# Kernel tuning notes

Measured on AMD Instinct MI355X. Metric: run time of the kernel, lower is better.

The kernel has to match this reference:

```python
import jax, jax.numpy as jnp
import numpy as np

D_MODEL = 256; N_HEADS = 8; N_LEVELS = 4; N_POINTS = 4; D_FFN = 1024
BS = 8; NQ = 100; NKPT = 17
LEVEL_SHAPES = [(160, 160), (80, 80), (40, 40), (20, 20)]  # (H, W) per level
LEN_V = sum(h * w for h, w in LEVEL_SHAPES)  # 34000


def layer_norm(x, g, b, eps=1e-5):
    m = x.mean(-1, keepdims=True)
    v = ((x - m) ** 2).mean(-1, keepdims=True)
    return (x - m) * jax.lax.rsqrt(v + eps) * g + b


def mha(q, k, v, Wqkv, bqkv, Wo, bo):
    # torch nn.MultiheadAttention, batch_first, eval mode (no dropout)
    d = q.shape[-1]; dh = d // N_HEADS
    def proj(x, W, b):
        return (x @ W.T + b).reshape(*x.shape[:-1], N_HEADS, dh)
    qp = proj(q, Wqkv[:d], bqkv[:d])
    kp = proj(k, Wqkv[d:2 * d], bqkv[d:2 * d])
    vp = proj(v, Wqkv[2 * d:], bqkv[2 * d:])
    att = jnp.einsum('bqhd,bkhd->bhqk', qp, kp) / jnp.sqrt(jnp.asarray(dh, q.dtype))
    att = jax.nn.softmax(att, -1)
    out = jnp.einsum('bhqk,bkhd->bqhd', att, vp).reshape(q.shape)
    return out @ Wo.T + bo


def bilinear_sample(val, loc, h, w):
    # val: (B, H, h*w, Dh); loc: (B, Lq, H, P, 2) normalized to [0,1]
    # matches F.grid_sample(align_corners=False, padding_mode='zeros') on grid 2*loc-1
    B, Lq, H, P, _ = loc.shape
    px = loc[..., 0] * w - 0.5
    py = loc[..., 1] * h - 0.5
    x0f = jnp.floor(px); y0f = jnp.floor(py)
    lx = px - x0f; ly = py - y0f
    x0 = x0f.astype(jnp.int32); y0 = y0f.astype(jnp.int32)
    out = jnp.zeros((B, H, Lq, P, val.shape[-1]), val.dtype)
    for dx, dy, wt in ((0, 0, (1 - lx) * (1 - ly)), (1, 0, lx * (1 - ly)),
                       (0, 1, (1 - lx) * ly), (1, 1, lx * ly)):
        xi = x0 + dx; yi = y0 + dy
        valid = ((xi >= 0) & (xi < w) & (yi >= 0) & (yi < h)).astype(val.dtype)
        idx = jnp.clip(yi, 0, h - 1) * w + jnp.clip(xi, 0, w - 1)  # (B,Lq,H,P)
        idx = idx.transpose(0, 2, 1, 3).reshape(B, H, Lq * P)
        g = jnp.take_along_axis(val, idx[..., None], axis=2).reshape(B, H, Lq, P, -1)
        out = out + g * (wt * valid).transpose(0, 2, 1, 3)[..., None]
    return out  # (B, H, Lq, P, Dh)


def ms_deform_attn(query, ref_points, memory, off_W, off_b, aw_W, aw_b,
                   val_W, val_b, outp_W, outp_b):
    B, Lq, _ = query.shape
    dh = D_MODEL // N_HEADS
    value = (memory @ val_W.T + val_b).reshape(B, LEN_V, N_HEADS, dh)
    off = (query @ off_W.T + off_b).reshape(B, Lq, N_HEADS, N_LEVELS, N_POINTS, 2)
    aw = (query @ aw_W.T + aw_b).reshape(B, Lq, N_HEADS, N_LEVELS * N_POINTS)
    aw = jax.nn.softmax(aw, -1).reshape(B, Lq, N_HEADS, N_LEVELS, N_POINTS)
    normalizer = jnp.array([[w, h] for h, w in LEVEL_SHAPES], dtype=query.dtype)  # (L,2) as (W,H)
    loc = ref_points[:, :, None, :, None, :] + off / normalizer[None, None, None, :, None, :]
    out = jnp.zeros((B, Lq, N_HEADS, dh), query.dtype)
    start = 0
    for l, (h, w) in enumerate(LEVEL_SHAPES):
        vl = value[:, start:start + h * w].transpose(0, 2, 1, 3)  # (B,H,hw,Dh)
        s = bilinear_sample(vl, loc[:, :, :, l], h, w)            # (B,H,Lq,P,Dh)
        out = out + jnp.einsum('bhqpd,bqhp->bqhd', s, aw[:, :, :, l])
        start += h * w
    return out.reshape(B, Lq, D_MODEL) @ outp_W.T + outp_b


def setup_inputs() -> dict:
    key = jax.random.key(0)
    ks = iter(jax.random.split(key, 40))
    d = D_MODEL
    def w(shape, s=0.02):
        return jax.random.normal(next(ks), shape, jnp.float32) * s
    inp = {
        'tgt_pose': jax.random.normal(next(ks), (BS, NQ, NKPT, d), jnp.float32),
        'tgt_pose_query_pos': jax.random.normal(next(ks), (BS, NQ, NKPT, d), jnp.float32),
        'tgt_pose_reference_points': jax.random.uniform(next(ks), (BS, NQ * NKPT, N_LEVELS, 2), jnp.float32),
        'memory': jax.random.normal(next(ks), (BS, LEN_V, d), jnp.float32),
        'win_Wqkv': w((3 * d, d)), 'win_bqkv': jnp.zeros((3 * d,), jnp.float32),
        'win_Wo': w((d, d)), 'win_bo': jnp.zeros((d,), jnp.float32),
        'win_ng': jnp.ones((d,), jnp.float32), 'win_nb': jnp.zeros((d,), jnp.float32),
        'acr_Wqkv': w((3 * d, d)), 'acr_bqkv': jnp.zeros((3 * d,), jnp.float32),
        'acr_Wo': w((d, d)), 'acr_bo': jnp.zeros((d,), jnp.float32),
        'acr_ng': jnp.ones((d,), jnp.float32), 'acr_nb': jnp.zeros((d,), jnp.float32),
        'off_W': w((N_HEADS * N_LEVELS * N_POINTS * 2, d)),
        'off_b': jax.random.uniform(next(ks), (N_HEADS * N_LEVELS * N_POINTS * 2,), jnp.float32, -1.0, 1.0),
        'aw_W': w((N_HEADS * N_LEVELS * N_POINTS, d)), 'aw_b': jnp.zeros((N_HEADS * N_LEVELS * N_POINTS,), jnp.float32),
        'val_W': w((d, d)), 'val_b': jnp.zeros((d,), jnp.float32),
        'outp_W': w((d, d)), 'outp_b': jnp.zeros((d,), jnp.float32),
        'gate_W': w((2 * d, 2 * d)), 'gate_b': jnp.zeros((2 * d,), jnp.float32),
        'gate_ng': jnp.ones((d,), jnp.float32), 'gate_nb': jnp.zeros((d,), jnp.float32),
        'ffn_W1': w((D_FFN, d)), 'ffn_b1': jnp.zeros((D_FFN,), jnp.float32),
        'ffn_W2': w((d, D_FFN)), 'ffn_b2': jnp.zeros((d,), jnp.float32),
        'n2_g': jnp.ones((d,), jnp.float32), 'n2_b': jnp.zeros((d,), jnp.float32),
        'memory_spatial_shapes': jnp.array(LEVEL_SHAPES, jnp.int32),
    }
    return inp


def reference(tgt_pose, tgt_pose_query_pos, tgt_pose_reference_points, memory,
              win_Wqkv, win_bqkv, win_Wo, win_bo, win_ng, win_nb,
              acr_Wqkv, acr_bqkv, acr_Wo, acr_bo, acr_ng, acr_nb,
              off_W, off_b, aw_W, aw_b, val_W, val_b, outp_W, outp_b,
              gate_W, gate_b, gate_ng, gate_nb,
              ffn_W1, ffn_b1, ffn_W2, ffn_b2, n2_g, n2_b,
              memory_spatial_shapes):
    bs, nq, K, d = tgt_pose.shape
    # with_pos_embed mutates tgt_pose in place in the torch code -> residual includes pos
    tgt = tgt_pose + tgt_pose_query_pos
    # within-attention over keypoints of each query
    x = tgt.reshape(bs * nq, K, d)
    t2 = mha(x, x, x, win_Wqkv, win_bqkv, win_Wo, win_bo).reshape(bs, nq, K, d)
    tgt = layer_norm(tgt + t2, win_ng, win_nb)
    # across-attention over queries for each keypoint
    xk = tgt.transpose(0, 2, 1, 3).reshape(bs * K, nq, d)
    t2 = mha(xk, xk, xk, acr_Wqkv, acr_bqkv, acr_Wo, acr_bo)
    tgt = layer_norm(xk + t2, acr_ng, acr_nb).reshape(bs, K, nq, d).transpose(0, 2, 1, 3)
    # second in-place pos add before deformable cross-attn (also feeds gateway)
    tgt_q = tgt + tgt_pose_query_pos
    t2 = ms_deform_attn(tgt_q.reshape(bs, nq * K, d), tgt_pose_reference_points, memory,
                        off_W, off_b, aw_W, aw_b, val_W, val_b, outp_W, outp_b)
    t2 = t2.reshape(bs, nq, K, d)
    # Gate
    g = jax.nn.sigmoid(jnp.concatenate([tgt_q, t2], -1) @ gate_W.T + gate_b)
    g1, g2 = jnp.split(g, 2, -1)
    tgt = layer_norm(g1 * tgt_q + g2 * t2, gate_ng, gate_nb)
    # FFN
    h = jax.nn.relu(tgt @ ffn_W1.T + ffn_b1)
    tgt = tgt + h @ ffn_W2.T + ffn_b2
    tgt = layer_norm(jnp.clip(tgt, -65504.0, 65504.0), n2_g, n2_b)
    return tgt
```

## Files before the change

kernel.cpp:

```cpp
#include <hip/hip_runtime.h>
#include <hip/hip_bf16.h>

#define NH 8
#define BS_ 8
#define NQ_ 100
#define NK_ 17
#define LQ 1700
#define T_TOK 13600
#define LEN_VV 34000

typedef __attribute__((ext_vector_type(8))) short short8v;
typedef __attribute__((ext_vector_type(8))) __bf16 bf16x8;
typedef __attribute__((ext_vector_type(4))) float f32x4;

__device__ __forceinline__ float wave_sum(float v){
#pragma unroll
  for (int m = 32; m; m >>= 1) v += __shfl_xor(v, m, 64);
  return v;
}
__device__ __forceinline__ short f2bf(float f){
  __hip_bfloat16 h = __float2bfloat16(f);
  return *reinterpret_cast<short*>(&h);
}

__global__ __launch_bounds__(256) void add_k(const float* __restrict__ a,
                                             const float* __restrict__ b,
                                             float* __restrict__ o, int n4){
  int i = blockIdx.x * 256 + threadIdx.x;
  if (i >= n4) return;
  float4 x = ((const float4*)a)[i];
  float4 y = ((const float4*)b)[i];
  float4 r; r.x = x.x + y.x; r.y = x.y + y.y; r.z = x.z + y.z; r.w = x.w + y.w;
  ((float4*)o)[i] = r;
}

__global__ __launch_bounds__(256) void transpose_k(const float* __restrict__ in,
                                                   float* __restrict__ outp){
  int i = blockIdx.x * 256 + threadIdx.x;
  if (i >= T_TOK * 64) return;
  int orow = i >> 6, c = i & 63;
  int b = orow / LQ, rem = orow % LQ;
  int kk = rem / NQ_, q = rem % NQ_;
  int irow = b * LQ + q * NK_ + kk;
  ((float4*)outp)[(size_t)orow * 64 + c] = ((const float4*)in)[(size_t)irow * 64 + c];
}

__global__ __launch_bounds__(256) void concat_k(const float* __restrict__ a,
                                                const float* __restrict__ b,
                                                float* __restrict__ o){
  int i = blockIdx.x * 256 + threadIdx.x;
  if (i >= T_TOK * 128) return;
  int row = i >> 7, c = i & 127;
  float4 v = (c < 64) ? ((const float4*)a)[(size_t)row * 64 + c]
                      : ((const float4*)b)[(size_t)row * 64 + (c - 64)];
  ((float4*)o)[(size_t)row * 128 + c] = v;
}

template<int EPI, int OUTB>
__global__ __launch_bounds__(256) void mgemm_k(const float* __restrict__ A,
                                               const float* __restrict__ W,
                                               const float* __restrict__ bias,
                                               float* __restrict__ Cf,
                                               __hip_bfloat16* __restrict__ Cb,
                                               int M, int N, int K){
  __shared__ short sh[OUTB ? 128 * 136 : 128 * 128];
  short* As = sh;
  short* Ws = sh + 128 * 64;
  const int tid = threadIdx.x;
  const int bm = blockIdx.y * 128, bn = blockIdx.x * 128;
  const int wave = tid >> 6, lane = tid & 63;
  const int wm = (wave >> 1) * 64, wn = (wave & 1) * 64;
  const int s = tid & 7;
  const int row0 = tid >> 3;
  f32x4 acc[4][4] = {};
  const int lrow = lane & 15, lk = lane >> 4;

  float4 ra[8], rw[8];
#pragma unroll
  for (int i = 0; i < 4; i++){
    int row = row0 + i * 32;
    int gr = bm + row;
    float4 z = make_float4(0.f, 0.f, 0.f, 0.f);
    if (gr < M){
      const float* p = A + (size_t)gr * K + s * 8;
      ra[2 * i] = ((const float4*)p)[0]; ra[2 * i + 1] = ((const float4*)p)[1];
    } else { ra[2 * i] = z; ra[2 * i + 1] = z; }
    const float* q = W + (size_t)(bn + row) * K + s * 8;
    rw[2 * i] = ((const float4*)q)[0]; rw[2 * i + 1] = ((const float4*)q)[1];
  }

  for (int k0 = 0; k0 < K; k0 += 64){
#pragma unroll
    for (int i = 0; i < 4; i++){
      int row = row0 + i * 32;
      int sw = ((s ^ (row & 7)) << 3) + row * 64;
      float4 a0 = ra[2 * i], a1 = ra[2 * i + 1];
      short8v v;
      v[0]=f2bf(a0.x); v[1]=f2bf(a0.y); v[2]=f2bf(a0.z); v[3]=f2bf(a0.w);
      v[4]=f2bf(a1.x); v[5]=f2bf(a1.y); v[6]=f2bf(a1.z); v[7]=f2bf(a1.w);
      *(short8v*)&As[sw] = v;
      a0 = rw[2 * i]; a1 = rw[2 * i + 1];
      short8v u;
      u[0]=f2bf(a0.x); u[1]=f2bf(a0.y); u[2]=f2bf(a0.z); u[3]=f2bf(a0.w);
      u[4]=f2bf(a1.x); u[5]=f2bf(a1.y); u[6]=f2bf(a1.z); u[7]=f2bf(a1.w);
      *(short8v*)&Ws[sw] = u;
    }
    __syncthreads();
    if (k0 + 64 < K){
#pragma unroll
      for (int i = 0; i < 4; i++){
        int row = row0 + i * 32;
        int gr = bm + row;
        float4 z = make_float4(0.f, 0.f, 0.f, 0.f);
        if (gr < M){
          const float* p = A + (size_t)gr * K + k0 + 64 + s * 8;
          ra[2 * i] = ((const float4*)p)[0]; ra[2 * i + 1] = ((const float4*)p)[1];
        } else { ra[2 * i] = z; ra[2 * i + 1] = z; }
        const float* q = W + (size_t)(bn + row) * K + k0 + 64 + s * 8;
        rw[2 * i] = ((const float4*)q)[0]; rw[2 * i + 1] = ((const float4*)q)[1];
      }
    }
#pragma unroll
    for (int ks = 0; ks < 2; ks++){
      short8v af[4], bw[4];
      int slot = ks * 4 + lk;
#pragma unroll
      for (int m = 0; m < 4; m++){
        int r = wm + m * 16 + lrow;
        af[m] = *(const short8v*)&As[r * 64 + ((slot ^ (r & 7)) << 3)];
      }
#pragma unroll
      for (int n = 0; n < 4; n++){
        int r = wn + n * 16 + lrow;
        bw[n] = *(const short8v*)&Ws[r * 64 + ((slot ^ (r & 7)) << 3)];
      }
#pragma unroll
      for (int m = 0; m < 4; m++)
#pragma unroll
        for (int n = 0; n < 4; n++)
          acc[m][n] = __builtin_amdgcn_mfma_f32_16x16x32_bf16(
              __builtin_bit_cast(bf16x8, af[m]),
              __builtin_bit_cast(bf16x8, bw[n]), acc[m][n], 0, 0, 0);
    }
    __syncthreads();
  }
  if (OUTB){
    const int STR = 136;
#pragma unroll
    for (int n = 0; n < 4; n++){
      int col = wn + n * 16 + lrow;
      float bsv = bias[bn + col];
#pragma unroll
      for (int m = 0; m < 4; m++){
#pragma unroll
        for (int i = 0; i < 4; i++){
          int row = wm + m * 16 + lk * 4 + i;
          float c = acc[m][n][i] + bsv;
          if (EPI == 1) c = fmaxf(c, 0.f);
          if (EPI == 2) c = 1.f / (1.f + expf(-c));
          sh[row * STR + col] = f2bf(c);
        }
      }
    }
    __syncthreads();
#pragma unroll
    for (int it = 0; it < 8; it++){
      int r = it * 16 + (tid >> 4);
      int chunk = tid & 15;
      if (bm + r < M){
        uint4 v = *(const uint4*)((const char*)sh + r * 272 + chunk * 16);
        *(uint4*)((char*)Cb + ((size_t)(bm + r) * N + bn) * 2 + chunk * 16) = v;
      }
    }
  } else {
#pragma unroll
    for (int n = 0; n < 4; n++){
      int col = bn + wn + n * 16 + lrow;
      float bsv = bias[col];
#pragma unroll
      for (int m = 0; m < 4; m++){
#pragma unroll
        for (int i = 0; i < 4; i++){
          int row = bm + wm + m * 16 + lk * 4 + i;
          if (row >= M) continue;
          float c = acc[m][n][i] + bsv;
          if (EPI == 1) c = fmaxf(c, 0.f);
          if (EPI == 2) c = 1.f / (1.f + expf(-c));
          Cf[(size_t)row * N + col] = c;
        }
      }
    }
  }
}

template<int TP>
__global__ __launch_bounds__(256) void mha_mfma_k(const float* __restrict__ qkv,
                                                  float* __restrict__ out, int S){
  constexpr int MT = TP / 16;
  constexpr int KSTEPS = (TP + 31) / 32;
  constexpr int KS32 = KSTEPS * 32;
  constexpr int VSTRB = (KS32 == 128) ? 256 : 128;
  __shared__ short QK[2][TP][64];
  __shared__ short Vt[2][32][VSTRB / 2];
  __shared__ float Sc[2][16][128];
  __shared__ float rinv[2][16];

  const int tid = threadIdx.x;
  const int bid = blockIdx.x;
  const int batch = bid >> 2, hp = bid & 3;
  const int wave = tid >> 6, lane = tid & 63;
  const int hh = wave >> 1, wsub = wave & 1;
  const int lrow = lane & 15, lk = lane >> 4;
  const float scale = 0.17677669529663687f;
  const size_t qbase = (size_t)batch * S * 768;

  for (int idx = tid; idx < 2 * TP * 4; idx += 256){
    int h2 = idx >= TP * 4;
    int rem = idx - h2 * TP * 4;
    int j = rem >> 2, s = rem & 3;
    int h = hp * 2 + h2;
    short8v qv = {}, kv = {};
    if (j < S){
      const float* p = qkv + qbase + (size_t)j * 768 + h * 32 + s * 8;
      float4 a = ((const float4*)p)[0];
      float4 b = ((const float4*)p)[1];
      qv[0]=f2bf(a.x*scale); qv[1]=f2bf(a.y*scale); qv[2]=f2bf(a.z*scale); qv[3]=f2bf(a.w*scale);
      qv[4]=f2bf(b.x*scale); qv[5]=f2bf(b.y*scale); qv[6]=f2bf(b.z*scale); qv[7]=f2bf(b.w*scale);
      float4 c = ((const float4*)(p + 256))[0];
      float4 d = ((const float4*)(p + 256))[1];
      kv[0]=f2bf(c.x); kv[1]=f2bf(c.y); kv[2]=f2bf(c.z); kv[3]=f2bf(c.w);
      kv[4]=f2bf(d.x); kv[5]=f2bf(d.y); kv[6]=f2bf(d.z); kv[7]=f2bf(d.w);
    }
    *(short8v*)&QK[h2][j][(s ^ (j & 7)) << 3] = qv;
    *(short8v*)&QK[h2][j][((s + 4) ^ (j & 7)) << 3] = kv;
  }
  for (int idx = tid; idx < 2 * KS32 * 8; idx += 256){
    int h2 = idx >= KS32 * 8;
    int rem = idx - h2 * KS32 * 8;
    int j = rem >> 3, e4 = rem & 7;
    int h = hp * 2 + h2;
    float4 v = make_float4(0.f, 0.f, 0.f, 0.f);
    if (j < S) v = *(const float4*)(qkv + qbase + (size_t)j * 768 + h * 32 + 512 + e4 * 4);
    short vs4[4] = { f2bf(v.x), f2bf(v.y), f2bf(v.z), f2bf(v.w) };
#pragma unroll
    for (int c = 0; c < 4; c++){
      int e = e4 * 4 + c;
      char* pb = (char*)&Vt[h2][0][0] + e * VSTRB + (((j >> 3) ^ (e & 7)) << 4) + ((j & 7) << 1);
      *(short*)pb = vs4[c];
    }
  }
  __syncthreads();

  for (int mt = 0; mt < MT; mt++){
    for (int nt = wsub; nt < MT; nt += 2){
      int ar = mt * 16 + lrow;
      short8v aq = *(const short8v*)&QK[hh][ar][(lk ^ (ar & 7)) << 3];
      int br = nt * 16 + lrow;
      short8v bk = *(const short8v*)&QK[hh][br][((lk + 4) ^ (br & 7)) << 3];
      f32x4 z = {};
      f32x4 d = __builtin_amdgcn_mfma_f32_16x16x32_bf16(
          __builtin_bit_cast(bf16x8, aq), __builtin_bit_cast(bf16x8, bk), z, 0, 0, 0);
#pragma unroll
      for (int i = 0; i < 4; i++){
        int rr = lk * 4 + i;
        int c = nt * 16 + lrow;
        Sc[hh][rr][(((c >> 2) ^ (rr & 7)) << 2) + (c & 3)] = d[i];
      }
    }
    __syncthreads();
    if (wsub == 0){
      int rr = lane >> 2, p = lane & 3;
      int grow = mt * 16 + rr;
      int Seff = (grow < S) ? S : 0;
      float mx = -1e30f;
#pragma unroll
      for (int m = 0; m < KSTEPS; m++){
        int j = p + 4 * m;
#pragma unroll
        for (int half = 0; half < 2; half++){
          int ls = 2 * j + half;
          float4 v = *(const float4*)&Sc[hh][rr][(ls ^ (rr & 7)) << 2];
          int c0 = ls * 4;
          mx = fmaxf(mx, (c0 + 0 < Seff) ? v.x : -1e30f);
          mx = fmaxf(mx, (c0 + 1 < Seff) ? v.y : -1e30f);
          mx = fmaxf(mx, (c0 + 2 < Seff) ? v.z : -1e30f);
          mx = fmaxf(mx, (c0 + 3 < Seff) ? v.w : -1e30f);
        }
      }
      mx = fmaxf(mx, __shfl_xor(mx, 1, 64));
      mx = fmaxf(mx, __shfl_xor(mx, 2, 64));
      float sum = 0.f;
#pragma unroll
      for (int m = 0; m < KSTEPS; m++){
        int j = p + 4 * m;
        float ev[8];
#pragma unroll
        for (int half = 0; half < 2; half++){
          int ls = 2 * j + half;
          float4 v = *(const float4*)&Sc[hh][rr][(ls ^ (rr & 7)) << 2];
          int c0 = ls * 4;
          ev[half * 4 + 0] = (c0 + 0 < Seff) ? __expf(v.x - mx) : 0.f;
          ev[half * 4 + 1] = (c0 + 1 < Seff) ? __expf(v.y - mx) : 0.f;
          ev[half * 4 + 2] = (c0 + 2 < Seff) ? __expf(v.z - mx) : 0.f;
          ev[half * 4 + 3] = (c0 + 3 < Seff) ? __expf(v.w - mx) : 0.f;
        }
        short8v pb;
#pragma unroll
        for (int q2 = 0; q2 < 8; q2++){ pb[q2] = f2bf(ev[q2]); sum += ev[q2]; }
        *(short8v*)((char*)&Sc[hh][rr][0] + ((j ^ (rr & 7)) << 4)) = pb;
      }
      sum += __shfl_xor(sum, 1, 64);
      sum += __shfl_xor(sum, 2, 64);
      if (p == 0) rinv[hh][rr] = (sum > 0.f) ? 1.f / sum : 0.f;
    }
    __syncthreads();
    {
      int nt2 = wsub;
      f32x4 acc = {};
#pragma unroll
      for (int ks = 0; ks < KSTEPS; ks++){
        int slot = ks * 4 + lk;
        short8v ap = *(const short8v*)((const char*)&Sc[hh][lrow][0] + ((slot ^ (lrow & 7)) << 4));
        int e = nt2 * 16 + lrow;
        short8v bv = *(const short8v*)((const char*)&Vt[hh][0][0] + e * VSTRB + ((slot ^ (e & 7)) << 4));
        acc = __builtin_amdgcn_mfma_f32_16x16x32_bf16(
            __builtin_bit_cast(bf16x8, ap), __builtin_bit_cast(bf16x8, bv), acc, 0, 0, 0);
      }
      int h = hp * 2 + hh;
#pragma unroll
      for (int i = 0; i < 4; i++){
        int row = mt * 16 + lk * 4 + i;
        if (row < S){
          float rv = rinv[hh][lk * 4 + i];
          out[((size_t)batch * S + row) * 256 + h * 32 + nt2 * 16 + lrow] = acc[i] * rv;
        }
      }
    }
    __syncthreads();
  }
}

template<int MODE>
__global__ __launch_bounds__(64) void ln_k(const float* __restrict__ a,
                                           const float* __restrict__ b,
                                           const float* __restrict__ g,
                                           const float* __restrict__ be,
                                           float* __restrict__ out){
  int r = blockIdx.x;
  int lane = threadIdx.x;
  float4 xa = *(const float4*)(a + (size_t)r * 256 + lane * 4);
  float4 xb = *(const float4*)(b + (size_t)r * 256 + lane * 4);
  float x[4] = { xa.x + xb.x, xa.y + xb.y, xa.z + xb.z, xa.w + xb.w };
  if (MODE == 2){
#pragma unroll
    for (int i = 0; i < 4; i++) x[i] = fminf(fmaxf(x[i], -65504.f), 65504.f);
  }
  float s = x[0] + x[1] + x[2] + x[3];
  s = wave_sum(s);
  float mean = s * (1.f / 256.f);
  float sq = 0.f;
#pragma unroll
  for (int i = 0; i < 4; i++){ float d = x[i] - mean; sq += d * d; }
  float var = wave_sum(sq) * (1.f / 256.f);
  float rstd = rsqrtf(var + 1e-5f);
  float4 gg = *(const float4*)(g + lane * 4);
  float4 bb = *(const float4*)(be + lane * 4);
  size_t orow = r;
  if (MODE == 1){
    int bi = r / LQ; int rem = r % LQ; int kk = rem / NQ_; int q = rem % NQ_;
    orow = (size_t)bi * LQ + q * NK_ + kk;
  }
  float4 o;
  o.x = (x[0] - mean) * rstd * gg.x + bb.x;
  o.y = (x[1] - mean) * rstd * gg.y + bb.y;
  o.z = (x[2] - mean) * rstd * gg.z + bb.z;
  o.w = (x[3] - mean) * rstd * gg.w + bb.w;
  *(float4*)(out + orow * 256 + lane * 4) = o;
}

__global__ __launch_bounds__(64) void gate_ln_k(const float* __restrict__ G,
                                                const float* __restrict__ aq,
                                                const float* __restrict__ t2,
                                                const float* __restrict__ g,
                                                const float* __restrict__ be,
                                                float* __restrict__ out){
  int r = blockIdx.x;
  int lane = threadIdx.x;
  float4 g1 = *(const float4*)(G + (size_t)r * 512 + lane * 4);
  float4 g2 = *(const float4*)(G + (size_t)r * 512 + 256 + lane * 4);
  float4 xa = *(const float4*)(aq + (size_t)r * 256 + lane * 4);
  float4 xt = *(const float4*)(t2 + (size_t)r * 256 + lane * 4);
  float x[4] = { g1.x * xa.x + g2.x * xt.x, g1.y * xa.y + g2.y * xt.y,
                 g1.z * xa.z + g2.z * xt.z, g1.w * xa.w + g2.w * xt.w };
  float s = x[0] + x[1] + x[2] + x[3];
  s = wave_sum(s);
  float mean = s * (1.f / 256.f);
  float sq = 0.f;
#pragma unroll
  for (int i = 0; i < 4; i++){ float d = x[i] - mean; sq += d * d; }
  float var = wave_sum(sq) * (1.f / 256.f);
  float rstd = rsqrtf(var + 1e-5f);
  float4 gg = *(const float4*)(g + lane * 4);
  float4 bb = *(const float4*)(be + lane * 4);
  float4 o;
  o.x = (x[0] - mean) * rstd * gg.x + bb.x;
  o.y = (x[1] - mean) * rstd * gg.y + bb.y;
  o.z = (x[2] - mean) * rstd * gg.z + bb.z;
  o.w = (x[3] - mean) * rstd * gg.w + bb.w;
  *(float4*)(out + (size_t)r * 256 + lane * 4) = o;
}

__global__ __launch_bounds__(256) void deform_k(const __hip_bfloat16* __restrict__ val,
                                                const float* __restrict__ off,
                                                const float* __restrict__ awr,
                                                const float* __restrict__ ref,
                                                float* __restrict__ out){
  __shared__ uint2 meta[32][16][4];
  const int tid = threadIdx.x;
  const int t0 = blockIdx.x * 4;
  {
    int g = tid >> 3;
    int pair = tid & 7;
    int lt = g >> 3, h = g & 7;
    int t = t0 + lt;
    int b = t / LQ;
    int p0 = pair * 2;
    int l = p0 >> 2;
    const int starts[4] = {0, 25600, 32000, 33600};
    const int HS[4] = {160, 80, 40, 20};
    int w = HS[l];
    float a0 = awr[(size_t)t * 128 + h * 16 + p0];
    float a1 = awr[(size_t)t * 128 + h * 16 + p0 + 1];
    float mx = fmaxf(a0, a1);
#pragma unroll
    for (int m = 1; m <= 4; m <<= 1) mx = fmaxf(mx, __shfl_xor(mx, m, 64));
    float e0 = expf(a0 - mx), e1 = expf(a1 - mx);
    float s = e0 + e1;
#pragma unroll
    for (int m = 1; m <= 4; m <<= 1) s += __shfl_xor(s, m, 64);
    float inv = 1.f / s;
    float rx = ref[((size_t)t * 4 + l) * 2 + 0];
    float ry = ref[((size_t)t * 4 + l) * 2 + 1];
    float4 ov = *(const float4*)(off + (size_t)t * 256 + h * 32 + l * 8 + p0 * 2);
    int vbase = (b * LEN_VV + starts[l]) * 128 + h * 16;
#pragma unroll
    for (int pp = 0; pp < 2; pp++){
      float wgt = (pp ? e1 : e0) * inv;
      float px = rx * w + (pp ? ov.z : ov.x) - 0.5f;
      float py = ry * w + (pp ? ov.w : ov.y) - 0.5f;
      float x0f = floorf(px), y0f = floorf(py);
      float lx = px - x0f, ly = py - y0f;
      int x0 = (int)x0f, y0 = (int)y0f;
#pragma unroll
      for (int c = 0; c < 4; c++){
        int dx = c & 1, dy = c >> 1;
        int xi = x0 + dx, yi = y0 + dy;
        bool ok = (xi >= 0) & (xi < w) & (yi >= 0) & (yi < w);
        float cw = ok ? wgt * (dx ? lx : 1.f - lx) * (dy ? ly : 1.f - ly) : 0.f;
        uint idx = ok ? (uint)(vbase + (yi * w + xi) * 128) : 0u;
        uint2 m2; m2.x = idx; m2.y = __float_as_uint(cw);
        meta[g][p0 + pp][c] = m2;
      }
    }
  }
  __syncthreads();
  const uint* V2 = (const uint*)val;
  int sg = tid >> 4, lane = tid & 15;
#pragma unroll
  for (int it = 0; it < 2; it++){
    int g = it * 16 + sg;
    int lt = g >> 3, h = g & 7;
    int t = t0 + lt;
    float ax = 0.f, ay = 0.f;
#pragma unroll 4
    for (int c = 0; c < 64; c++){
      uint2 mw = meta[g][c >> 2][c & 3];
      float wv = __uint_as_float(mw.y);
      uint v = V2[(size_t)mw.x + lane];
      float lo = __uint_as_float(v << 16);
      float hi = __uint_as_float(v & 0xffff0000u);
      ax += wv * lo;
      ay += wv * hi;
    }
    float2 r; r.x = ax; r.y = ay;
    *(float2*)(out + (size_t)t * 256 + h * 32 + lane * 2) = r;
  }
}

extern "C" void kernel_launch(void* const* d_in, const int* in_sizes, int n_in,
                              void* d_out, int out_size, void* d_ws, size_t ws_size,
                              hipStream_t stream){
  const float* tgt_pose = (const float*)d_in[0];
  const float* qpos     = (const float*)d_in[1];
  const float* refp     = (const float*)d_in[2];
  const float* memory   = (const float*)d_in[3];
  const float* win_Wqkv = (const float*)d_in[4];
  const float* win_bqkv = (const float*)d_in[5];
  const float* win_Wo   = (const float*)d_in[6];
  const float* win_bo   = (const float*)d_in[7];
  const float* win_ng   = (const float*)d_in[8];
  const float* win_nb   = (const float*)d_in[9];
  const float* acr_Wqkv = (const float*)d_in[10];
  const float* acr_bqkv = (const float*)d_in[11];
  const float* acr_Wo   = (const float*)d_in[12];
  const float* acr_bo   = (const float*)d_in[13];
  const float* acr_ng   = (const float*)d_in[14];
  const float* acr_nb   = (const float*)d_in[15];
  const float* off_W    = (const float*)d_in[16];
  const float* off_b    = (const float*)d_in[17];
  const float* aw_W     = (const float*)d_in[18];
  const float* aw_b     = (const float*)d_in[19];
  const float* val_W    = (const float*)d_in[20];
  const float* val_b    = (const float*)d_in[21];
  const float* outp_W   = (const float*)d_in[22];
  const float* outp_b   = (const float*)d_in[23];
  const float* gate_W   = (const float*)d_in[24];
  const float* gate_b   = (const float*)d_in[25];
  const float* gate_ng  = (const float*)d_in[26];
  const float* gate_nb  = (const float*)d_in[27];
  const float* ffn_W1   = (const float*)d_in[28];
  const float* ffn_b1   = (const float*)d_in[29];
  const float* ffn_W2   = (const float*)d_in[30];
  const float* ffn_b2   = (const float*)d_in[31];
  const float* n2_g     = (const float*)d_in[32];
  const float* n2_b     = (const float*)d_in[33];

  float* out = (float*)d_out;
  char* ws = (char*)d_ws;
  const size_t TB = (size_t)T_TOK * 256 * 4;
  float* B0 = (float*)(ws);
  float* B1 = (float*)(ws + TB);
  float* B2 = (float*)(ws + 2 * TB);
  float* B3 = (float*)(ws + 3 * TB);
  float* Q  = (float*)(ws + 4 * TB);
  float* AW = (float*)(ws + 4 * TB + (size_t)T_TOK * 768 * 4);
  char*  Vb = ws + 4 * TB + (size_t)T_TOK * 768 * 4 + (size_t)T_TOK * 128 * 4;
  __hip_bfloat16* V = (__hip_bfloat16*)Vb;
  float* CAT = (float*)Vb;
  float* FF  = (float*)(Vb + (size_t)T_TOK * 512 * 4);

  const int n4 = T_TOK * 64;
  const int GM = (T_TOK + 127) / 128;

  add_k<<<(n4 + 255) / 256, 256, 0, stream>>>(tgt_pose, qpos, B0, n4);
  mgemm_k<0,0><<<dim3(6, GM), 256, 0, stream>>>(B0, win_Wqkv, win_bqkv, Q, nullptr, T_TOK, 768, 256);
  mha_mfma_k<32><<<800 * 4, 256, 0, stream>>>(Q, B1, 17);
  mgemm_k<0,0><<<dim3(2, GM), 256, 0, stream>>>(B1, win_Wo, win_bo, B2, nullptr, T_TOK, 256, 256);
  ln_k<0><<<T_TOK, 64, 0, stream>>>(B0, B2, win_ng, win_nb, B1);
  transpose_k<<<(n4 + 255) / 256, 256, 0, stream>>>(B1, B0);
  mgemm_k<0,0><<<dim3(6, GM), 256, 0, stream>>>(B0, acr_Wqkv, acr_bqkv, Q, nullptr, T_TOK, 768, 256);
  mha_mfma_k<112><<<136 * 4, 256, 0, stream>>>(Q, B2, 100);
  mgemm_k<0,0><<<dim3(2, GM), 256, 0, stream>>>(B2, acr_Wo, acr_bo, B3, nullptr, T_TOK, 256, 256);
  ln_k<1><<<T_TOK, 64, 0, stream>>>(B0, B3, acr_ng, acr_nb, B1);
  add_k<<<(n4 + 255) / 256, 256, 0, stream>>>(B1, qpos, B0, n4);
  mgemm_k<0,1><<<dim3(2, 2125), 256, 0, stream>>>(memory, val_W, val_b, nullptr, V, BS_ * LEN_VV, 256, 256);
  mgemm_k<0,0><<<dim3(2, GM), 256, 0, stream>>>(B0, off_W, off_b, B1, nullptr, T_TOK, 256, 256);
  mgemm_k<0,0><<<dim3(1, GM), 256, 0, stream>>>(B0, aw_W, aw_b, AW, nullptr, T_TOK, 128, 256);
  deform_k<<<T_TOK / 4, 256, 0, stream>>>(V, B1, AW, refp, B2);
  mgemm_k<0,0><<<dim3(2, GM), 256, 0, stream>>>(B2, outp_W, outp_b, B3, nullptr, T_TOK, 256, 256);
  concat_k<<<(T_TOK * 128 + 255) / 256, 256, 0, stream>>>(B0, B3, CAT);
  mgemm_k<2,0><<<dim3(4, GM), 256, 0, stream>>>(CAT, gate_W, gate_b, Q, nullptr, T_TOK, 512, 512);
  gate_ln_k<<<T_TOK, 64, 0, stream>>>(Q, B0, B3, gate_ng, gate_nb, B1);
  mgemm_k<1,0><<<dim3(8, GM), 256, 0, stream>>>(B1, ffn_W1, ffn_b1, FF, nullptr, T_TOK, 1024, 256);
  mgemm_k<0,0><<<dim3(2, GM), 256, 0, stream>>>(FF, ffn_W2, ffn_b2, B2, nullptr, T_TOK, 256, 1024);
  ln_k<2><<<T_TOK, 64, 0, stream>>>(B1, B2, n2_g, n2_b, out);
}
```

Before: 571.2 us.

## Fuse transposes, concat and projections; use bf16 intermediates and 64-tile GEMMs

```diff
diff --git a/kernel.cpp b/kernel.cpp
--- a/kernel.cpp
+++ b/kernel.cpp
@@ -21,6 +21,9 @@
 __device__ __forceinline__ short f2bf(float f){
   __hip_bfloat16 h = __float2bfloat16(f);
   return *reinterpret_cast<short*>(&h);
+}
+__device__ __forceinline__ float bf2f(short s){
+  return __uint_as_float(((uint)(unsigned short)s) << 16);
 }
 
 __global__ __launch_bounds__(256) void add_k(const float* __restrict__ a,
@@ -32,28 +35,6 @@
   float4 y = ((const float4*)b)[i];
   float4 r; r.x = x.x + y.x; r.y = x.y + y.y; r.z = x.z + y.z; r.w = x.w + y.w;
   ((float4*)o)[i] = r;
-}
-
-__global__ __launch_bounds__(256) void transpose_k(const float* __restrict__ in,
-                                                   float* __restrict__ outp){
-  int i = blockIdx.x * 256 + threadIdx.x;
-  if (i >= T_TOK * 64) return;
-  int orow = i >> 6, c = i & 63;
-  int b = orow / LQ, rem = orow % LQ;
-  int kk = rem / NQ_, q = rem % NQ_;
-  int irow = b * LQ + q * NK_ + kk;
-  ((float4*)outp)[(size_t)orow * 64 + c] = ((const float4*)in)[(size_t)irow * 64 + c];
-}
-
-__global__ __launch_bounds__(256) void concat_k(const float* __restrict__ a,
-                                                const float* __restrict__ b,
-                                                float* __restrict__ o){
-  int i = blockIdx.x * 256 + threadIdx.x;
-  if (i >= T_TOK * 128) return;
-  int row = i >> 7, c = i & 127;
-  float4 v = (c < 64) ? ((const float4*)a)[(size_t)row * 64 + c]
-                      : ((const float4*)b)[(size_t)row * 64 + (c - 64)];
-  ((float4*)o)[(size_t)row * 128 + c] = v;
 }
 
 template<int EPI, int OUTB>
@@ -193,9 +174,138 @@
   }
 }
 
+template<int EPI, int OUTB, int INB, int DUALA>
+__global__ __launch_bounds__(256) void g64_k(const void* __restrict__ Av,
+                                             const void* __restrict__ A1v,
+                                             const float* __restrict__ W0,
+                                             const float* __restrict__ W1,
+                                             int NSPLIT,
+                                             const float* __restrict__ bias0,
+                                             const float* __restrict__ bias1,
+                                             float* __restrict__ Cf,
+                                             __hip_bfloat16* __restrict__ Cb,
+                                             int M, int N, int K, int sA){
+  __shared__ short sh64[2 * 64 * 64];
+  short* As = sh64;
+  short* Ws = sh64 + 64 * 64;
+  const int tid = threadIdx.x;
+  const int bn = blockIdx.x * 64, bm = blockIdx.y * 64;
+  const int wave = tid >> 6, lane = tid & 63;
+  const int wm = (wave >> 1) * 32, wn = (wave & 1) * 32;
+  const int s = tid & 7, row0 = tid >> 3;
+  const int lrow = lane & 15, lk = lane >> 4;
+  f32x4 acc[2][2] = {};
+
+  for (int k0 = 0; k0 < K; k0 += 64){
+#pragma unroll
+    for (int i = 0; i < 2; i++){
+      int row = row0 + i * 32;
+      int sw = ((s ^ (row & 7)) << 3) + row * 64;
+      short8v v = {};
+      int gr = bm + row;
+      if (gr < M){
+        if (INB){
+          v = *(const short8v*)((const short*)Av + (size_t)gr * sA + k0 + s * 8);
+        } else {
+          const float* Ap;
+          if (DUALA) Ap = (k0 < 256) ? (const float*)Av + (size_t)gr * 256 + k0
+                                     : (const float*)A1v + (size_t)gr * 256 + (k0 - 256);
+          else Ap = (const float*)Av + (size_t)gr * sA + k0;
+          float4 a0 = ((const float4*)(Ap + s * 8))[0];
+          float4 a1 = ((const float4*)(Ap + s * 8))[1];
+          v[0]=f2bf(a0.x); v[1]=f2bf(a0.y); v[2]=f2bf(a0.z); v[3]=f2bf(a0.w);
+          v[4]=f2bf(a1.x); v[5]=f2bf(a1.y); v[6]=f2bf(a1.z); v[7]=f2bf(a1.w);
+        }
+      }
+      *(short8v*)&As[sw] = v;
+      int wr = bn + row;
+      const float* Wp = (wr < NSPLIT) ? W0 + (size_t)wr * K + k0
+                                      : W1 + (size_t)(wr - NSPLIT) * K + k0;
+      float4 b0 = ((const float4*)(Wp + s * 8))[0];
+      float4 b1 = ((const float4*)(Wp + s * 8))[1];
+      short8v u;
+      u[0]=f2bf(b0.x); u[1]=f2bf(b0.y); u[2]=f2bf(b0.z); u[3]=f2bf(b0.w);
+      u[4]=f2bf(b1.x); u[5]=f2bf(b1.y); u[6]=f2bf(b1.z); u[7]=f2bf(b1.w);
+      *(short8v*)&Ws[sw] = u;
+    }
+    __syncthreads();
+#pragma unroll
+    for (int ks = 0; ks < 2; ks++){
+      int slot = ks * 4 + lk;
+      short8v af[2], bw[2];
+#pragma unroll
+      for (int m = 0; m < 2; m++){
+        int r = wm + m * 16 + lrow;
+        af[m] = *(const short8v*)&As[r * 64 + ((slot ^ (r & 7)) << 3)];
+      }
+#pragma unroll
+      for (int n = 0; n < 2; n++){
+        int r = wn + n * 16 + lrow;
+        bw[n] = *(const short8v*)&Ws[r * 64 + ((slot ^ (r & 7)) << 3)];
+      }
+#pragma unroll
+      for (int m = 0; m < 2; m++)
+#pragma unroll
+        for (int n = 0; n < 2; n++)
+          acc[m][n] = __builtin_amdgcn_mfma_f32_16x16x32_bf16(
+              __builtin_bit_cast(bf16x8, af[m]),
+              __builtin_bit_cast(bf16x8, bw[n]), acc[m][n], 0, 0, 0);
+    }
+    __syncthreads();
+  }
+  if (OUTB){
+    const int STR = 72;
+#pragma unroll
+    for (int n = 0; n < 2; n++){
+      int col = wn + n * 16 + lrow;
+      int gc = bn + col;
+      float bsv = (gc < NSPLIT) ? bias0[gc] : bias1[gc - NSPLIT];
+#pragma unroll
+      for (int m = 0; m < 2; m++){
+#pragma unroll
+        for (int i = 0; i < 4; i++){
+          int row = wm + m * 16 + lk * 4 + i;
+          float c = acc[m][n][i] + bsv;
+          if (EPI == 1) c = fmaxf(c, 0.f);
+          if (EPI == 2) c = 1.f / (1.f + expf(-c));
+          sh64[row * STR + col] = f2bf(c);
+        }
+      }
+    }
+    __syncthreads();
+#pragma unroll
+    for (int it = 0; it < 2; it++){
+      int r = it * 32 + (tid >> 3);
+      int chunk = tid & 7;
+      if (bm + r < M){
+        uint4 v = *(const uint4*)((const char*)sh64 + r * 144 + chunk * 16);
+        *(uint4*)((char*)Cb + ((size_t)(bm + r) * N + bn) * 2 + chunk * 16) = v;
+      }
+    }
+  } else {
+#pragma unroll
+    for (int n = 0; n < 2; n++){
+      int gc = bn + wn + n * 16 + lrow;
+      float bsv = (gc < NSPLIT) ? bias0[gc] : bias1[gc - NSPLIT];
+#pragma unroll
+      for (int m = 0; m < 2; m++){
+#pragma unroll
+        for (int i = 0; i < 4; i++){
+          int row = bm + wm + m * 16 + lk * 4 + i;
+          if (row >= M) continue;
+          float c = acc[m][n][i] + bsv;
+          if (EPI == 1) c = fmaxf(c, 0.f);
+          if (EPI == 2) c = 1.f / (1.f + expf(-c));
+          Cf[(size_t)row * N + gc] = c;
+        }
+      }
+    }
+  }
+}
+
 template<int TP>
-__global__ __launch_bounds__(256) void mha_mfma_k(const float* __restrict__ qkv,
-                                                  float* __restrict__ out, int S){
+__global__ __launch_bounds__(256) void mha_mfma_k(const short* __restrict__ qkv,
+                                                  __hip_bfloat16* __restrict__ out, int S){
   constexpr int MT = TP / 16;
   constexpr int KSTEPS = (TP + 31) / 32;
   constexpr int KS32 = KSTEPS * 32;
@@ -221,32 +331,25 @@
     int h = hp * 2 + h2;
     short8v qv = {}, kv = {};
     if (j < S){
-      const float* p = qkv + qbase + (size_t)j * 768 + h * 32 + s * 8;
-      float4 a = ((const float4*)p)[0];
-      float4 b = ((const float4*)p)[1];
-      qv[0]=f2bf(a.x*scale); qv[1]=f2bf(a.y*scale); qv[2]=f2bf(a.z*scale); qv[3]=f2bf(a.w*scale);
-      qv[4]=f2bf(b.x*scale); qv[5]=f2bf(b.y*scale); qv[6]=f2bf(b.z*scale); qv[7]=f2bf(b.w*scale);
-      float4 c = ((const float4*)(p + 256))[0];
-      float4 d = ((const float4*)(p + 256))[1];
-      kv[0]=f2bf(c.x); kv[1]=f2bf(c.y); kv[2]=f2bf(c.z); kv[3]=f2bf(c.w);
-      kv[4]=f2bf(d.x); kv[5]=f2bf(d.y); kv[6]=f2bf(d.z); kv[7]=f2bf(d.w);
+      const short* p = qkv + qbase + (size_t)j * 768 + h * 32 + s * 8;
+      qv = *(const short8v*)p;
+      kv = *(const short8v*)(p + 256);
     }
     *(short8v*)&QK[h2][j][(s ^ (j & 7)) << 3] = qv;
     *(short8v*)&QK[h2][j][((s + 4) ^ (j & 7)) << 3] = kv;
   }
-  for (int idx = tid; idx < 2 * KS32 * 8; idx += 256){
-    int h2 = idx >= KS32 * 8;
-    int rem = idx - h2 * KS32 * 8;
-    int j = rem >> 3, e4 = rem & 7;
+  for (int idx = tid; idx < 2 * KS32 * 4; idx += 256){
+    int h2 = idx >= KS32 * 4;
+    int rem = idx - h2 * KS32 * 4;
+    int j = rem >> 2, e8 = rem & 3;
     int h = hp * 2 + h2;
-    float4 v = make_float4(0.f, 0.f, 0.f, 0.f);
-    if (j < S) v = *(const float4*)(qkv + qbase + (size_t)j * 768 + h * 32 + 512 + e4 * 4);
-    short vs4[4] = { f2bf(v.x), f2bf(v.y), f2bf(v.z), f2bf(v.w) };
-#pragma unroll
-    for (int c = 0; c < 4; c++){
-      int e = e4 * 4 + c;
+    short8v v = {};
+    if (j < S) v = *(const short8v*)(qkv + qbase + (size_t)j * 768 + h * 32 + 512 + e8 * 8);
+#pragma unroll
+    for (int c = 0; c < 8; c++){
+      int e = e8 * 8 + c;
       char* pb = (char*)&Vt[h2][0][0] + e * VSTRB + (((j >> 3) ^ (e & 7)) << 4) + ((j & 7) << 1);
-      *(short*)pb = vs4[c];
+      *(short*)pb = v[c];
     }
   }
   __syncthreads();
@@ -264,7 +367,7 @@
       for (int i = 0; i < 4; i++){
         int rr = lk * 4 + i;
         int c = nt * 16 + lrow;
-        Sc[hh][rr][(((c >> 2) ^ (rr & 7)) << 2) + (c & 3)] = d[i];
+        Sc[hh][rr][(((c >> 2) ^ (rr & 7)) << 2) + (c & 3)] = d[i] * scale;
       }
     }
     __syncthreads();
@@ -332,7 +435,8 @@
         int row = mt * 16 + lk * 4 + i;
         if (row < S){
           float rv = rinv[hh][lk * 4 + i];
-          out[((size_t)batch * S + row) * 256 + h * 32 + nt2 * 16 + lrow] = acc[i] * rv;
+          out[((size_t)batch * S + row) * 256 + h * 32 + nt2 * 16 + lrow] =
+              __float2bfloat16(acc[i] * rv);
         }
       }
     }
@@ -345,7 +449,8 @@
                                            const float* __restrict__ b,
                                            const float* __restrict__ g,
                                            const float* __restrict__ be,
-                                           float* __restrict__ out){
+                                           float* __restrict__ out,
+                                           const float* __restrict__ qp){
   int r = blockIdx.x;
   int lane = threadIdx.x;
   float4 xa = *(const float4*)(a + (size_t)r * 256 + lane * 4);
@@ -366,19 +471,27 @@
   float4 gg = *(const float4*)(g + lane * 4);
   float4 bb = *(const float4*)(be + lane * 4);
   size_t orow = r;
-  if (MODE == 1){
+  if (MODE == 3){
     int bi = r / LQ; int rem = r % LQ; int kk = rem / NQ_; int q = rem % NQ_;
     orow = (size_t)bi * LQ + q * NK_ + kk;
+  }
+  if (MODE == 4){
+    int bi = r / LQ; int rem = r % LQ; int q = rem / NK_; int kk = rem % NK_;
+    orow = (size_t)bi * LQ + kk * NQ_ + q;
   }
   float4 o;
   o.x = (x[0] - mean) * rstd * gg.x + bb.x;
   o.y = (x[1] - mean) * rstd * gg.y + bb.y;
   o.z = (x[2] - mean) * rstd * gg.z + bb.z;
   o.w = (x[3] - mean) * rstd * gg.w + bb.w;
+  if (MODE == 3){
+    float4 qv = *(const float4*)(qp + orow * 256 + lane * 4);
+    o.x += qv.x; o.y += qv.y; o.z += qv.z; o.w += qv.w;
+  }
   *(float4*)(out + orow * 256 + lane * 4) = o;
 }
 
-__global__ __launch_bounds__(64) void gate_ln_k(const float* __restrict__ G,
+__global__ __launch_bounds__(64) void gate_ln_k(const short* __restrict__ G,
                                                 const float* __restrict__ aq,
                                                 const float* __restrict__ t2,
                                                 const float* __restrict__ g,
@@ -386,12 +499,14 @@
                                                 float* __restrict__ out){
   int r = blockIdx.x;
   int lane = threadIdx.x;
-  float4 g1 = *(const float4*)(G + (size_t)r * 512 + lane * 4);
-  float4 g2 = *(const float4*)(G + (size_t)r * 512 + 256 + lane * 4);
+  const short* gp = G + (size_t)r * 512 + lane * 4;
+  float g1v[4], g2v[4];
+#pragma unroll
+  for (int i = 0; i < 4; i++){ g1v[i] = bf2f(gp[i]); g2v[i] = bf2f(gp[256 + i]); }
   float4 xa = *(const float4*)(aq + (size_t)r * 256 + lane * 4);
   float4 xt = *(const float4*)(t2 + (size_t)r * 256 + lane * 4);
-  float x[4] = { g1.x * xa.x + g2.x * xt.x, g1.y * xa.y + g2.y * xt.y,
-                 g1.z * xa.z + g2.z * xt.z, g1.w * xa.w + g2.w * xt.w };
+  float x[4] = { g1v[0] * xa.x + g2v[0] * xt.x, g1v[1] * xa.y + g2v[1] * xt.y,
+                 g1v[2] * xa.z + g2v[2] * xt.z, g1v[3] * xa.w + g2v[3] * xt.w };
   float s = x[0] + x[1] + x[2] + x[3];
   s = wave_sum(s);
   float mean = s * (1.f / 256.f);
@@ -411,10 +526,9 @@
 }
 
 __global__ __launch_bounds__(256) void deform_k(const __hip_bfloat16* __restrict__ val,
-                                                const float* __restrict__ off,
-                                                const float* __restrict__ awr,
+                                                const float* __restrict__ offaw,
                                                 const float* __restrict__ ref,
-                                                float* __restrict__ out){
+                                                unsigned int* __restrict__ outb){
   __shared__ uint2 meta[32][16][4];
   const int tid = threadIdx.x;
   const int t0 = blockIdx.x * 4;
@@ -429,8 +543,9 @@
     const int starts[4] = {0, 25600, 32000, 33600};
     const int HS[4] = {160, 80, 40, 20};
     int w = HS[l];
-    float a0 = awr[(size_t)t * 128 + h * 16 + p0];
-    float a1 = awr[(size_t)t * 128 + h * 16 + p0 + 1];
+    const float* ap = offaw + (size_t)t * 384 + 256 + h * 16;
+    float a0 = ap[p0];
+    float a1 = ap[p0 + 1];
     float mx = fmaxf(a0, a1);
 #pragma unroll
     for (int m = 1; m <= 4; m <<= 1) mx = fmaxf(mx, __shfl_xor(mx, m, 64));
@@ -441,7 +556,7 @@
     float inv = 1.f / s;
     float rx = ref[((size_t)t * 4 + l) * 2 + 0];
     float ry = ref[((size_t)t * 4 + l) * 2 + 1];
-    float4 ov = *(const float4*)(off + (size_t)t * 256 + h * 32 + l * 8 + p0 * 2);
+    float4 ov = *(const float4*)(offaw + (size_t)t * 384 + h * 32 + l * 8 + p0 * 2);
     int vbase = (b * LEN_VV + starts[l]) * 128 + h * 16;
 #pragma unroll
     for (int pp = 0; pp < 2; pp++){
@@ -482,8 +597,8 @@
       ax += wv * lo;
       ay += wv * hi;
     }
-    float2 r; r.x = ax; r.y = ay;
-    *(float2*)(out + (size_t)t * 256 + h * 32 + lane * 2) = r;
+    uint u = ((uint)(unsigned short)f2bf(ay) << 16) | (uint)(unsigned short)f2bf(ax);
+    outb[((size_t)t * 256 + h * 32) / 2 + lane] = u;
   }
 }
 
@@ -532,36 +647,36 @@
   float* B1 = (float*)(ws + TB);
   float* B2 = (float*)(ws + 2 * TB);
   float* B3 = (float*)(ws + 3 * TB);
-  float* Q  = (float*)(ws + 4 * TB);
-  float* AW = (float*)(ws + 4 * TB + (size_t)T_TOK * 768 * 4);
-  char*  Vb = ws + 4 * TB + (size_t)T_TOK * 768 * 4 + (size_t)T_TOK * 128 * 4;
-  __hip_bfloat16* V = (__hip_bfloat16*)Vb;
-  float* CAT = (float*)Vb;
-  float* FF  = (float*)(Vb + (size_t)T_TOK * 512 * 4);
+  char* p = ws + 4 * TB;
+  short* Qb = (short*)p;                 p += (size_t)T_TOK * 768 * 2;
+  short* ABF = (short*)p;                p += (size_t)T_TOK * 256 * 2;
+  float* OFFAW = (float*)p;              p += (size_t)T_TOK * 384 * 4;
+  short* Gb = (short*)p;                 p += (size_t)T_TOK * 512 * 2;
+  char* Vregion = p;
+  __hip_bfloat16* V = (__hip_bfloat16*)Vregion;
+  short* FF = (short*)Vregion;
 
   const int n4 = T_TOK * 64;
-  const int GM = (T_TOK + 127) / 128;
+  const int GM128 = (T_TOK + 127) / 128;
+  const int GM64  = (T_TOK + 63) / 64;
+  const int BIG = 1 << 30;
 
   add_k<<<(n4 + 255) / 256, 256, 0, stream>>>(tgt_pose, qpos, B0, n4);
-  mgemm_k<0,0><<<dim3(6, GM), 256, 0, stream>>>(B0, win_Wqkv, win_bqkv, Q, nullptr, T_TOK, 768, 256);
-  mha_mfma_k<32><<<800 * 4, 256, 0, stream>>>(Q, B1, 17);
-  mgemm_k<0,0><<<dim3(2, GM), 256, 0, stream>>>(B1, win_Wo, win_bo, B2, nullptr, T_TOK, 256, 256);
-  ln_k<0><<<T_TOK, 64, 0, stream>>>(B0, B2, win_ng, win_nb, B1);
-  transpose_k<<<(n4 + 255) / 256, 256, 0, stream>>>(B1, B0);
-  mgemm_k<0,0><<<dim3(6, GM), 256, 0, stream>>>(B0, acr_Wqkv, acr_bqkv, Q, nullptr, T_TOK, 768, 256);
-  mha_mfma_k<112><<<136 * 4, 256, 0, stream>>>(Q, B2, 100);
-  mgemm_k<0,0><<<dim3(2, GM), 256, 0, stream>>>(B2, acr_Wo, acr_bo, B3, nullptr, T_TOK, 256, 256);
-  ln_k<1><<<T_TOK, 64, 0, stream>>>(B0, B3, acr_ng, acr_nb, B1);
-  add_k<<<(n4 + 255) / 256, 256, 0, stream>>>(B1, qpos, B0, n4);
+  mgemm_k<0,1><<<dim3(6, GM128), 256, 0, stream>>>(B0, win_Wqkv, win_bqkv, nullptr, (__hip_bfloat16*)Qb, T_TOK, 768, 256);
+  mha_mfma_k<32><<<800 * 4, 256, 0, stream>>>(Qb, (__hip_bfloat16*)ABF, 17);
+  g64_k<0,0,1,0><<<dim3(4, GM64), 256, 0, stream>>>(ABF, nullptr, win_Wo, win_Wo, BIG, win_bo, win_bo, B2, nullptr, T_TOK, 256, 256, 256);
+  ln_k<4><<<T_TOK, 64, 0, stream>>>(B0, B2, win_ng, win_nb, B1, nullptr);
+  mgemm_k<0,1><<<dim3(6, GM128), 256, 0, stream>>>(B1, acr_Wqkv, acr_bqkv, nullptr, (__hip_bfloat16*)Qb, T_TOK, 768, 256);
+  mha_mfma_k<112><<<136 * 4, 256, 0, stream>>>(Qb, (__hip_bfloat16*)ABF, 100);
+  g64_k<0,0,1,0><<<dim3(4, GM64), 256, 0, stream>>>(ABF, nullptr, acr_Wo, acr_Wo, BIG, acr_bo, acr_bo, B2, nullptr, T_TOK, 256, 256, 256);
+  ln_k<3><<<T_TOK, 64, 0, stream>>>(B1, B2, acr_ng, acr_nb, B0, qpos);
   mgemm_k<0,1><<<dim3(2, 2125), 256, 0, stream>>>(memory, val_W, val_b, nullptr, V, BS_ * LEN_VV, 256, 256);
-  mgemm_k<0,0><<<dim3(2, GM), 256, 0, stream>>>(B0, off_W, off_b, B1, nullptr, T_TOK, 256, 256);
-  mgemm_k<0,0><<<dim3(1, GM), 256, 0, stream>>>(B0, aw_W, aw_b, AW, nullptr, T_TOK, 128, 256);
-  deform_k<<<T_TOK / 4, 256, 0, stream>>>(V, B1, AW, refp, B2);
-  mgemm_k<0,0><<<dim3(2, GM), 256, 0, stream>>>(B2, outp_W, outp_b, B3, nullptr, T_TOK, 256, 256);
-  concat_k<<<(T_TOK * 128 + 255) / 256, 256, 0, stream>>>(B0, B3, CAT);
-  mgemm_k<2,0><<<dim3(4, GM), 256, 0, stream>>>(CAT, gate_W, gate_b, Q, nullptr, T_TOK, 512, 512);
-  gate_ln_k<<<T_TOK, 64, 0, stream>>>(Q, B0, B3, gate_ng, gate_nb, B1);
-  mgemm_k<1,0><<<dim3(8, GM), 256, 0, stream>>>(B1, ffn_W1, ffn_b1, FF, nullptr, T_TOK, 1024, 256);
-  mgemm_k<0,0><<<dim3(2, GM), 256, 0, stream>>>(FF, ffn_W2, ffn_b2, B2, nullptr, T_TOK, 256, 1024);
-  ln_k<2><<<T_TOK, 64, 0, stream>>>(B1, B2, n2_g, n2_b, out);
-}
+  g64_k<0,0,0,0><<<dim3(6, GM64), 256, 0, stream>>>(B0, nullptr, off_W, aw_W, 256, off_b, aw_b, OFFAW, nullptr, T_TOK, 384, 256, 256);
+  deform_k<<<T_TOK / 4, 256, 0, stream>>>(V, OFFAW, refp, (unsigned int*)ABF);
+  g64_k<0,0,1,0><<<dim3(4, GM64), 256, 0, stream>>>(ABF, nullptr, outp_W, outp_W, BIG, outp_b, outp_b, B3, nullptr, T_TOK, 256, 256, 256);
+  g64_k<2,1,0,1><<<dim3(8, GM64), 256, 0, stream>>>(B0, B3, gate_W, gate_W, BIG, gate_b, gate_b, nullptr, (__hip_bfloat16*)Gb, T_TOK, 512, 512, 256);
+  gate_ln_k<<<T_TOK, 64, 0, stream>>>(Gb, B0, B3, gate_ng, gate_nb, B2);
+  mgemm_k<1,1><<<dim3(8, GM128), 256, 0, stream>>>(B2, ffn_W1, ffn_b1, nullptr, (__hip_bfloat16*)FF, T_TOK, 1024, 256);
+  g64_k<0,0,1,0><<<dim3(4, GM64), 256, 0, stream>>>(FF, nullptr, ffn_W2, ffn_W2, BIG, ffn_b2, ffn_b2, B1, nullptr, T_TOK, 256, 1024, 1024);
+  ln_k<2><<<T_TOK, 64, 0, stream>>>(B2, B1, n2_g, n2_b, out, nullptr);
+}
```

Result: faster. 465.4 us (-18.5%).
